# Performance work log

Hardware: AMD Instinct MI355X
Metric: run time of the kernel (lower is better)

## Reference

```python
import jax, jax.numpy as jnp
import numpy as np

EPS = 1e-6

def _normalize(A):
    # zero the diagonal, add self-loops
    n = A.shape[-1]
    eye = jnp.eye(n, dtype=A.dtype)
    A_hat = A * (1.0 - eye) + eye  # [B,N,N]
    # symmetric degree normalization with eps inside as in the TF code:
    # d = 1/(eps + sqrt(rowsum)); norm = diag(d) @ A_hat @ diag(d)
    d = 1.0 / (EPS + jnp.sqrt(jnp.sum(A_hat, axis=2)))  # [B,N]
    return A_hat * d[:, :, None] * d[:, None, :]


def setup_inputs() -> dict:
    key = jax.random.key(0)
    k1, k2, k3 = jax.random.split(key, 3)
    B, N, F, O = 8, 2048, 128, 128
    x = jax.random.normal(k1, (B, N, F), dtype=jnp.float32)
    adj = jax.random.uniform(k2, (B, N, N), dtype=jnp.float32)
    kernel = jax.random.normal(k3, (F, O), dtype=jnp.float32) * 0.05
    return {"x": x, "adj": adj, "kernel": kernel}


def reference(x, adj, kernel):
    norm = _normalize(adj)                      # [B,N,N]
    agg = jnp.einsum('bnm,bmf->bnf', norm, x)   # batch_dot
    out = jnp.einsum('bnf,fo->bno', agg, kernel)
    return jax.nn.relu(out)
```

## Files before the change

### kernel.cpp

```cpp
#include <hip/hip_runtime.h>


typedef __bf16 bf16x8 __attribute__((ext_vector_type(8)));
typedef __bf16 bf16x4 __attribute__((ext_vector_type(4)));
typedef float  f32x4  __attribute__((ext_vector_type(4)));

#define NN 2048
#define NB 8

__device__ __forceinline__ void load_lds16(__bf16* lds, const __bf16* g) {
    __builtin_amdgcn_global_load_lds(
        (const __attribute__((address_space(1))) void*)g,
        (__attribute__((address_space(3))) void*)lds, 16, 0, 0);
}

__global__ __launch_bounds__(256) void wt_kernel(const float* __restrict__ W,
                                                 __bf16* __restrict__ Wt) {
    int idx = blockIdx.x * 256 + threadIdx.x;
    int f = idx >> 7, o = idx & 127;
    Wt[o * 128 + f] = (__bf16)W[idx];
}

__global__ __launch_bounds__(256) void d_kernel(const float* __restrict__ adj,
                                                float* __restrict__ dvec) {
    const int lane = threadIdx.x & 63;
    const int row  = blockIdx.x * 4 + (threadIdx.x >> 6);
    const float* rp = adj + (size_t)row * NN;
    float4 s4 = {0.f, 0.f, 0.f, 0.f};
#pragma unroll
    for (int it = 0; it < 8; ++it) {
        float4 v = *(const float4*)(rp + it * 256 + lane * 4);
        s4.x += v.x; s4.y += v.y; s4.z += v.z; s4.w += v.w;
    }
    float s = (s4.x + s4.y) + (s4.z + s4.w);
#pragma unroll
    for (int off = 32; off; off >>= 1) s += __shfl_down(s, off);
    if (lane == 0) {
        int n = row & (NN - 1);
        float sh = s - rp[n] + 1.0f;
        dvec[row] = 1.0f / (1e-6f + sqrtf(sh));
    }
}

template <int KTOT, bool IS_XW>
__global__ __launch_bounds__(256) void gemm_kernel(
    const float* __restrict__ A, const __bf16* __restrict__ Bmat,
    const float* __restrict__ dvec, float* __restrict__ out,
    __bf16* __restrict__ yt) {
    __shared__ alignas(16) __bf16 sA[2][32][40];
    __shared__ alignas(16) __bf16 sB[2][128][32];

    const int tid  = threadIdx.x;
    const int wave = tid >> 6;
    const int lane = tid & 63;
    const int b    = blockIdx.x & 7;
    const int tile = blockIdx.x >> 3;
    const int n_local_base = tile * 32;
    const int row_base = b * NN + n_local_base;

    const __bf16* Bptr = IS_XW ? Bmat : (Bmat + (size_t)b * 128 * KTOT);

    const int a_row = tid >> 3;
    const int a_col = (tid & 7) * 4;
    const float* a_src = A + (size_t)(row_base + a_row) * KTOT + a_col;

    const int b_row0 = wave * 32;
    const __bf16* b_src =
        Bptr + (size_t)(b_row0 + (lane >> 2)) * KTOT + (lane & 3) * 8;

    const int rsel = (wave & 1) * 16;
    const int csel = (wave >> 1) * 64;

    f32x4 acc[4];
#pragma unroll
    for (int i = 0; i < 4; ++i) acc[i] = (f32x4){0.f, 0.f, 0.f, 0.f};

    f32x4 a = *(const f32x4*)(a_src);
    load_lds16(&sB[0][b_row0][0], b_src);
    load_lds16(&sB[0][b_row0 + 16][0], b_src + (size_t)16 * KTOT);

    const int NITER = KTOT / 32;
    for (int kt = 0; kt < NITER; ++kt) {
        const int cur = kt & 1;
        float av[4] = {a.x, a.y, a.z, a.w};
        if constexpr (!IS_XW) {
            int n  = n_local_base + a_row;
            int m0 = kt * 32 + a_col;
#pragma unroll
            for (int j = 0; j < 4; ++j)
                if (m0 + j == n) av[j] = 1.0f;
        }
        bf16x4 apack;
#pragma unroll
        for (int j = 0; j < 4; ++j) apack[j] = (__bf16)av[j];
        *(bf16x4*)(&sA[cur][a_row][a_col]) = apack;

        __syncthreads();

        if (kt + 1 < NITER) {
            const __bf16* bs = b_src + (size_t)(kt + 1) * 32;
            load_lds16(&sB[cur ^ 1][b_row0][0], bs);
            load_lds16(&sB[cur ^ 1][b_row0 + 16][0], bs + (size_t)16 * KTOT);
            a = *(const f32x4*)(a_src + (size_t)(kt + 1) * 32);
        }

        bf16x8 af = *(const bf16x8*)(&sA[cur][rsel + (lane & 15)][(lane >> 4) * 8]);
#pragma unroll
        for (int nb = 0; nb < 4; ++nb) {
            bf16x8 bfv = *(const bf16x8*)(
                &sB[cur][csel + nb * 16 + (lane & 15)][(lane >> 4) * 8]);
            acc[nb] = __builtin_amdgcn_mfma_f32_16x16x32_bf16(af, bfv, acc[nb], 0, 0, 0);
        }
    }

    const int col0 = lane & 15;
    const int rq   = (lane >> 4) * 4;
#pragma unroll
    for (int r = 0; r < 4; ++r) {
        int grow = row_base + rsel + rq + r;
        float dr = dvec[grow];
        if constexpr (IS_XW) {
            int m_loc = grow - b * NN;
#pragma unroll
            for (int nb = 0; nb < 4; ++nb) {
                int o = csel + nb * 16 + col0;
                yt[((size_t)b * 128 + o) * NN + m_loc] = (__bf16)(acc[nb][r] * dr);
            }
        } else {
#pragma unroll
            for (int nb = 0; nb < 4; ++nb) {
                int o = csel + nb * 16 + col0;
                float v = acc[nb][r] * dr;
                out[(size_t)grow * 128 + o] = v > 0.f ? v : 0.f;
            }
        }
    }
}

extern "C" void kernel_launch(void* const* d_in, const int* in_sizes, int n_in,
                              void* d_out, int out_size, void* d_ws, size_t ws_size,
                              hipStream_t stream) {
    const float* x   = (const float*)d_in[0];
    const float* adj = (const float*)d_in[1];
    const float* W   = (const float*)d_in[2];
    float* out = (float*)d_out;

    char* ws = (char*)d_ws;
    float*  dvec = (float*)ws;
    __bf16* yt   = (__bf16*)(ws + 65536);
    __bf16* Wt   = (__bf16*)(ws + 65536 + (size_t)NB * 128 * NN * 2);

    hipLaunchKernelGGL(wt_kernel, dim3(64), dim3(256), 0, stream, W, Wt);
    hipLaunchKernelGGL(d_kernel, dim3(NB * NN / 4), dim3(256), 0, stream, adj, dvec);
    hipLaunchKernelGGL((gemm_kernel<128, true>), dim3(512), dim3(256), 0, stream,
                       x, Wt, dvec, (float*)nullptr, yt);
    hipLaunchKernelGGL((gemm_kernel<2048, false>), dim3(512), dim3(256), 0, stream,
                       adj, yt, dvec, out, (__bf16*)nullptr);
}
```

Before: 249.2 us.

## Pre-convert scaled adjacency to bf16 in degree pass, drop LDS staging in GEMMs

The degree kernel now also writes a bf16 copy of the adjacency with the diagonal replaced and rows pre-scaled by d. The main GEMM then streams half-size bf16 operands straight from global memory into MFMA registers, with no LDS, no barriers and no per-element diagonal fix. The XW GEMM is rewritten in the same register-direct style. The trade is an extra 64MB bf16 write plus re-read against the fp32 adjacency read inside the GEMM, and the loss of LDS reuse, so the B operand is re-fetched per wave and leans on cache.

Result: slower. 288.7 us (+15.9%).

```diff
diff --git a/kernel.cpp b/kernel.cpp
--- a/kernel.cpp
+++ b/kernel.cpp
@@ -8,12 +8,6 @@
 #define NN 2048
 #define NB 8
 
-__device__ __forceinline__ void load_lds16(__bf16* lds, const __bf16* g) {
-    __builtin_amdgcn_global_load_lds(
-        (const __attribute__((address_space(1))) void*)g,
-        (__attribute__((address_space(3))) void*)lds, 16, 0, 0);
-}
-
 __global__ __launch_bounds__(256) void wt_kernel(const float* __restrict__ W,
                                                  __bf16* __restrict__ Wt) {
     int idx = blockIdx.x * 256 + threadIdx.x;
@@ -21,118 +15,133 @@
     Wt[o * 128 + f] = (__bf16)W[idx];
 }
 
-__global__ __launch_bounds__(256) void d_kernel(const float* __restrict__ adj,
-                                                float* __restrict__ dvec) {
+__global__ __launch_bounds__(256) void prep_kernel(const float* __restrict__ adj,
+                                                   float* __restrict__ dvec,
+                                                   __bf16* __restrict__ adjb) {
     const int lane = threadIdx.x & 63;
     const int row  = blockIdx.x * 4 + (threadIdx.x >> 6);
     const float* rp = adj + (size_t)row * NN;
-    float4 s4 = {0.f, 0.f, 0.f, 0.f};
+    __bf16* wp = adjb + (size_t)row * NN;
+    const int n = row & (NN - 1);
+
+    f32x4 v[8];
+    float s = 0.f;
 #pragma unroll
     for (int it = 0; it < 8; ++it) {
-        float4 v = *(const float4*)(rp + it * 256 + lane * 4);
-        s4.x += v.x; s4.y += v.y; s4.z += v.z; s4.w += v.w;
+        v[it] = *(const f32x4*)(rp + it * 256 + lane * 4);
+        s += (v[it].x + v[it].y) + (v[it].z + v[it].w);
     }
-    float s = (s4.x + s4.y) + (s4.z + s4.w);
 #pragma unroll
-    for (int off = 32; off; off >>= 1) s += __shfl_down(s, off);
-    if (lane == 0) {
-        int n = row & (NN - 1);
-        float sh = s - rp[n] + 1.0f;
-        dvec[row] = 1.0f / (1e-6f + sqrtf(sh));
+    for (int off = 1; off < 64; off <<= 1) s += __shfl_xor(s, off);
+    float diag = rp[n];
+    float d = 1.0f / (1e-6f + sqrtf(s - diag + 1.0f));
+    if (lane == 0) dvec[row] = d;
+
+#pragma unroll
+    for (int it = 0; it < 8; ++it) {
+        int c0 = it * 256 + lane * 4;
+        float f0 = (c0     == n) ? 1.0f : v[it].x;
+        float f1 = (c0 + 1 == n) ? 1.0f : v[it].y;
+        float f2 = (c0 + 2 == n) ? 1.0f : v[it].z;
+        float f3 = (c0 + 3 == n) ? 1.0f : v[it].w;
+        bf16x4 o4;
+        o4[0] = (__bf16)(f0 * d); o4[1] = (__bf16)(f1 * d);
+        o4[2] = (__bf16)(f2 * d); o4[3] = (__bf16)(f3 * d);
+        *(bf16x4*)(wp + c0) = o4;
     }
 }
 
-template <int KTOT, bool IS_XW>
-__global__ __launch_bounds__(256) void gemm_kernel(
-    const float* __restrict__ A, const __bf16* __restrict__ Bmat,
-    const float* __restrict__ dvec, float* __restrict__ out,
-    __bf16* __restrict__ yt) {
-    __shared__ alignas(16) __bf16 sA[2][32][40];
-    __shared__ alignas(16) __bf16 sB[2][128][32];
+__global__ __launch_bounds__(256) void xw_kernel(const float* __restrict__ x,
+                                                 const __bf16* __restrict__ Wt,
+                                                 const float* __restrict__ dvec,
+                                                 __bf16* __restrict__ yt) {
+    const int lane = threadIdx.x & 63;
+    const int wave = threadIdx.x >> 6;
+    const int b    = blockIdx.x & 7;
+    const int mt   = (blockIdx.x >> 3) * 4 + wave;
+    const int m0   = mt * 16;
+    const int kgrp = (lane >> 4) * 8;
+    const float* xp = x + ((size_t)b * NN + m0 + (lane & 15)) * 128 + kgrp;
 
-    const int tid  = threadIdx.x;
-    const int wave = tid >> 6;
-    const int lane = tid & 63;
+    f32x4 acc[8];
+#pragma unroll
+    for (int i = 0; i < 8; ++i) acc[i] = (f32x4){0.f, 0.f, 0.f, 0.f};
+
+#pragma unroll
+    for (int kt = 0; kt < 4; ++kt) {
+        f32x4 a0 = *(const f32x4*)(xp + kt * 32);
+        f32x4 a1 = *(const f32x4*)(xp + kt * 32 + 4);
+        float av[8] = {a0.x, a0.y, a0.z, a0.w, a1.x, a1.y, a1.z, a1.w};
+        bf16x8 af;
+#pragma unroll
+        for (int j = 0; j < 8; ++j) af[j] = (__bf16)av[j];
+#pragma unroll
+        for (int nb = 0; nb < 8; ++nb) {
+            bf16x8 bfv = *(const bf16x8*)(Wt + (nb * 16 + (lane & 15)) * 128 +
+                                          kt * 32 + kgrp);
+            acc[nb] = __builtin_amdgcn_mfma_f32_16x16x32_bf16(af, bfv, acc[nb], 0, 0, 0);
+        }
+    }
+    const int col0 = lane & 15;
+    const int rq   = (lane >> 4) * 4;
+#pragma unroll
+    for (int r = 0; r < 4; ++r) {
+        int m = m0 + rq + r;
+        float dm = dvec[b * NN + m];
+#pragma unroll
+        for (int nb = 0; nb < 8; ++nb) {
+            int o = nb * 16 + col0;
+            yt[((size_t)b * 128 + o) * NN + m] = (__bf16)(acc[nb][r] * dm);
+        }
+    }
+}
+
+__global__ __launch_bounds__(256) void gemm_kernel(const __bf16* __restrict__ adjb,
+                                                   const __bf16* __restrict__ yt,
+                                                   float* __restrict__ out) {
+    const int lane = threadIdx.x & 63;
+    const int wave = threadIdx.x >> 6;
     const int b    = blockIdx.x & 7;
     const int tile = blockIdx.x >> 3;
-    const int n_local_base = tile * 32;
-    const int row_base = b * NN + n_local_base;
-
-    const __bf16* Bptr = IS_XW ? Bmat : (Bmat + (size_t)b * 128 * KTOT);
-
-    const int a_row = tid >> 3;
-    const int a_col = (tid & 7) * 4;
-    const float* a_src = A + (size_t)(row_base + a_row) * KTOT + a_col;
-
-    const int b_row0 = wave * 32;
-    const __bf16* b_src =
-        Bptr + (size_t)(b_row0 + (lane >> 2)) * KTOT + (lane & 3) * 8;
-
     const int rsel = (wave & 1) * 16;
     const int csel = (wave >> 1) * 64;
+    const int kgrp = (lane >> 4) * 8;
+
+    const __bf16* ap =
+        adjb + ((size_t)b * NN + tile * 32 + rsel + (lane & 15)) * NN + kgrp;
+    const __bf16* bbase = yt + (size_t)b * 128 * NN + kgrp;
+    const __bf16* bp0 = bbase + (size_t)(csel + 0 * 16 + (lane & 15)) * NN;
+    const __bf16* bp1 = bbase + (size_t)(csel + 1 * 16 + (lane & 15)) * NN;
+    const __bf16* bp2 = bbase + (size_t)(csel + 2 * 16 + (lane & 15)) * NN;
+    const __bf16* bp3 = bbase + (size_t)(csel + 3 * 16 + (lane & 15)) * NN;
 
     f32x4 acc[4];
 #pragma unroll
     for (int i = 0; i < 4; ++i) acc[i] = (f32x4){0.f, 0.f, 0.f, 0.f};
 
-    f32x4 a = *(const f32x4*)(a_src);
-    load_lds16(&sB[0][b_row0][0], b_src);
-    load_lds16(&sB[0][b_row0 + 16][0], b_src + (size_t)16 * KTOT);
-
-    const int NITER = KTOT / 32;
-    for (int kt = 0; kt < NITER; ++kt) {
-        const int cur = kt & 1;
-        float av[4] = {a.x, a.y, a.z, a.w};
-        if constexpr (!IS_XW) {
-            int n  = n_local_base + a_row;
-            int m0 = kt * 32 + a_col;
-#pragma unroll
-            for (int j = 0; j < 4; ++j)
-                if (m0 + j == n) av[j] = 1.0f;
-        }
-        bf16x4 apack;
-#pragma unroll
-        for (int j = 0; j < 4; ++j) apack[j] = (__bf16)av[j];
-        *(bf16x4*)(&sA[cur][a_row][a_col]) = apack;
-
-        __syncthreads();
-
-        if (kt + 1 < NITER) {
-            const __bf16* bs = b_src + (size_t)(kt + 1) * 32;
-            load_lds16(&sB[cur ^ 1][b_row0][0], bs);
-            load_lds16(&sB[cur ^ 1][b_row0 + 16][0], bs + (size_t)16 * KTOT);
-            a = *(const f32x4*)(a_src + (size_t)(kt + 1) * 32);
-        }
-
-        bf16x8 af = *(const bf16x8*)(&sA[cur][rsel + (lane & 15)][(lane >> 4) * 8]);
-#pragma unroll
-        for (int nb = 0; nb < 4; ++nb) {
-            bf16x8 bfv = *(const bf16x8*)(
-                &sB[cur][csel + nb * 16 + (lane & 15)][(lane >> 4) * 8]);
-            acc[nb] = __builtin_amdgcn_mfma_f32_16x16x32_bf16(af, bfv, acc[nb], 0, 0, 0);
-        }
+#pragma unroll 4
+    for (int kt = 0; kt < 64; ++kt) {
+        const int ko = kt * 32;
+        bf16x8 af  = *(const bf16x8*)(ap  + ko);
+        bf16x8 bf0 = *(const bf16x8*)(bp0 + ko);
+        bf16x8 bf1 = *(const bf16x8*)(bp1 + ko);
+        bf16x8 bf2 = *(const bf16x8*)(bp2 + ko);
+        bf16x8 bf3 = *(const bf16x8*)(bp3 + ko);
+        acc[0] = __builtin_amdgcn_mfma_f32_16x16x32_bf16(af, bf0, acc[0], 0, 0, 0);
+        acc[1] = __builtin_amdgcn_mfma_f32_16x16x32_bf16(af, bf1, acc[1], 0, 0, 0);
+        acc[2] = __builtin_amdgcn_mfma_f32_16x16x32_bf16(af, bf2, acc[2], 0, 0, 0);
+        acc[3] = __builtin_amdgcn_mfma_f32_16x16x32_bf16(af, bf3, acc[3], 0, 0, 0);
     }
 
     const int col0 = lane & 15;
     const int rq   = (lane >> 4) * 4;
+    float* op = out + ((size_t)b * NN + tile * 32 + rsel) * 128;
 #pragma unroll
     for (int r = 0; r < 4; ++r) {
-        int grow = row_base + rsel + rq + r;
-        float dr = dvec[grow];
-        if constexpr (IS_XW) {
-            int m_loc = grow - b * NN;
 #pragma unroll
-            for (int nb = 0; nb < 4; ++nb) {
-                int o = csel + nb * 16 + col0;
-                yt[((size_t)b * 128 + o) * NN + m_loc] = (__bf16)(acc[nb][r] * dr);
-            }
-        } else {
-#pragma unroll
-            for (int nb = 0; nb < 4; ++nb) {
-                int o = csel + nb * 16 + col0;
-                float v = acc[nb][r] * dr;
-                out[(size_t)grow * 128 + o] = v > 0.f ? v : 0.f;
-            }
+        for (int nb = 0; nb < 4; ++nb) {
+            float v = acc[nb][r];
+            op[(rq + r) * 128 + csel + nb * 16 + col0] = v > 0.f ? v : 0.f;
         }
     }
 }
@@ -147,13 +156,15 @@
 
     char* ws = (char*)d_ws;
     float*  dvec = (float*)ws;
-    __bf16* yt   = (__bf16*)(ws + 65536);
-    __bf16* Wt   = (__bf16*)(ws + 65536 + (size_t)NB * 128 * NN * 2);
+    __bf16* Wt   = (__bf16*)(ws + (64 << 10));
+    __bf16* yt   = (__bf16*)(ws + (128 << 10));
+    __bf16* adjb = (__bf16*)(ws + (128 << 10) + ((size_t)NB * 128 * NN * 2));
 
     hipLaunchKernelGGL(wt_kernel, dim3(64), dim3(256), 0, stream, W, Wt);
-    hipLaunchKernelGGL(d_kernel, dim3(NB * NN / 4), dim3(256), 0, stream, adj, dvec);
-    hipLaunchKernelGGL((gemm_kernel<128, true>), dim3(512), dim3(256), 0, stream,
-                       x, Wt, dvec, (float*)nullptr, yt);
-    hipLaunchKernelGGL((gemm_kernel<2048, false>), dim3(512), dim3(256), 0, stream,
-                       adj, yt, dvec, out, (__bf16*)nullptr);
+    hipLaunchKernelGGL(prep_kernel, dim3(NB * NN / 4), dim3(256), 0, stream,
+                       adj, dvec, adjb);
+    hipLaunchKernelGGL(xw_kernel, dim3(256), dim3(256), 0, stream,
+                       x, Wt, dvec, yt);
+    hipLaunchKernelGGL(gemm_kernel, dim3(512), dim3(256), 0, stream,
+                       adjb, yt, out);
 }
```
